# Optimization experiments

Hardware: AMD Instinct MI355X
Metric: run time of the kernel (lower is better)

## Reference

```python
import jax, jax.numpy as jnp
import numpy as np

RADII = (0.4, 0.8, 1.2)
SIGMA2 = 2.0 * 0.2 ** 2   # Gaussian shell-density bandwidth
ALPHA = 0.3               # keras LeakyReLU default
EPS = 1e-3                # keras BatchNormalization default epsilon


def _n_coeffs(L):
    return sum((2 * l + 1) ** 2 for l in range(L + 1))


def _pullback_idx(L):
    # flat index of Wigner block entry (m, n=0) for each SH coeff (l, m)
    idx, off = [], 0
    for l in range(L + 1):
        d = 2 * l + 1
        idx += [off + m * d + l for m in range(d)]
        off += d * d
    return np.asarray(idx, dtype=np.int32)


def setup_inputs() -> dict:
    key = jax.random.key(0)
    ks = jax.random.split(key, 20)
    B, N, Q, S = 64, 2048, 1024, 512
    T = [_n_coeffs(l) for l in (5, 4, 3)]  # 286, 165, 84
    f32 = jnp.float32

    def nrm(k, shape, scale=1.0):
        return jax.random.normal(ks[k], shape, dtype=f32) * scale

    dirs = nrm(1, (3, S, 3))
    dirs = dirs / jnp.linalg.norm(dirs, axis=-1, keepdims=True)
    z = lambda n: jnp.zeros((n,), f32)
    o = lambda n: jnp.ones((n,), f32)
    return {
        "x": nrm(0, (B, N, 3)),
        "shell_dirs": dirs,                                   # [3, 512, 3]
        "A_sh": nrm(2, (36, S), 1.0 / np.sqrt(S)),            # SH projection (l_max=5)
        "D_eval0": nrm(3, (Q, T[0]), 1.0 / np.sqrt(T[0])),    # Wigner eval bases
        "D_eval1": nrm(4, (Q, T[1]), 1.0 / np.sqrt(T[1])),
        "D_eval2": nrm(5, (Q, T[2]), 1.0 / np.sqrt(T[2])),
        "D_coef1": nrm(6, (T[1], Q), 1.0 / np.sqrt(Q)),       # Wigner coeff (projection) bases
        "D_coef2": nrm(7, (T[2], Q), 1.0 / np.sqrt(Q)),
        "D_coef_last": nrm(8, (T[2], Q), 1.0 / np.sqrt(Q)),
        "W0": nrm(9, (3, 16), 1.0 / np.sqrt(3)), "b0": z(16),
        "W1": nrm(10, (16, 32), 0.25), "b1": z(32),
        "W2": nrm(11, (32, 64), 1.0 / np.sqrt(32)), "b2": z(64),
        "g0": o(16), "be0": z(16),
        "g1": o(32), "be1": z(32),
        "g2": o(64), "be2": z(64),
        "Wfc1": nrm(12, (256, 512), 1.0 / 16.0), "bfc1": z(512),
        "gfc1": o(512), "befc1": z(512),
        "Wfc2": nrm(13, (512, 256), 1.0 / np.sqrt(512)), "bfc2": z(256),
        "gfc2": o(256), "befc2": z(256),
        "Wout": nrm(14, (256, 40), 1.0 / 16.0), "bout": z(40),
    }


def _bn(y, g, b, axes):
    m = jnp.mean(y, axis=axes, keepdims=True)
    v = jnp.var(y, axis=axes, keepdims=True)
    return (y - m) * jax.lax.rsqrt(v + EPS) * g + b


def reference(x, shell_dirs, A_sh, D_eval0, D_eval1, D_eval2,
              D_coef1, D_coef2, D_coef_last,
              W0, b0, W1, b1, W2, b2,
              g0, be0, g1, be1, g2, be2,
              Wfc1, bfc1, gfc1, befc1, Wfc2, bfc2, gfc2, befc2,
              Wout, bout):
    B = x.shape[0]
    # --- sphere_shell_embedding: Gaussian shell density -> SH coeffs per shell ---
    xn2 = jnp.sum(x * x, -1)[..., None]                 # [B,N,1]
    sh = []
    for i, r in enumerate(RADII):
        c = r * shell_dirs[i]                           # [S,3]
        d2 = xn2 + jnp.sum(c * c, -1) - 2.0 * (x @ c.T)  # [B,N,S]
        f = jnp.mean(jnp.exp(-d2 / SIGMA2), axis=1)      # [B,S]
        sh.append(f @ A_sh.T)                            # [B,36]
    sh = jnp.stack(sh, axis=-1)                          # [B,36,3] shells as channels
    # --- S2_to_SO3_pullback: Y_lm -> D^l_{m,0} column of Wigner blocks ---
    idx = jnp.asarray(_pullback_idx(5))
    y = jnp.zeros((B, 286, 3), sh.dtype).at[:, idx, :].set(sh)
    # --- layer 0: SO3Conv (per-coeff channel mix) + WignerEval + BN + LReLU + WignerCoeffs ---
    y = jnp.einsum('btc,cu->btu', y, W0) + b0
    y = jnp.einsum('qt,btu->bqu', D_eval0, y)            # [B,1024,16]
    y = jax.nn.leaky_relu(_bn(y, g0, be0, (0, 1)), ALPHA)
    y = jnp.einsum('tq,bqu->btu', D_coef1, y)            # [B,165,16]
    # --- layer 1 ---
    y = jnp.einsum('btc,cu->btu', y, W1) + b1
    y = jnp.einsum('qt,btu->bqu', D_eval1, y)            # [B,1024,32]
    y = jax.nn.leaky_relu(_bn(y, g1, be1, (0, 1)), ALPHA)
    y = jnp.einsum('tq,bqu->btu', D_coef2, y)            # [B,84,32]
    # --- layer 2 ---
    y = jnp.einsum('btc,cu->btu', y, W2) + b2
    y = jnp.einsum('qt,btu->bqu', D_eval2, y)            # [B,1024,64]
    y = jax.nn.leaky_relu(_bn(y, g2, be2, (0, 1)), ALPHA)
    y = jnp.einsum('tq,bqu->btu', D_coef_last, y)        # [B,84,64]
    # --- degree-wise norms (rotation-invariant pooling), l_max=3 blocks ---
    offs, sizes = (0, 1, 10, 35), (1, 9, 25, 49)
    feats = jnp.concatenate(
        [jnp.linalg.norm(y[:, o:o + s, :], axis=1, keepdims=True)
         for o, s in zip(offs, sizes)], axis=1)          # [B,4,64]
    h = feats.reshape(B, -1)                             # [B,256]
    # --- MLP head (dropout = identity at inference) ---
    h = jax.nn.relu(_bn(h @ Wfc1 + bfc1, gfc1, befc1, (0,)))
    h = jax.nn.relu(_bn(h @ Wfc2 + bfc2, gfc2, befc2, (0,)))
    return jax.nn.softmax(h @ Wout + bout, axis=-1)
```

## Files before the change

### kernel.cpp

```cpp
#include <hip/hip_runtime.h>
#include <hip/hip_bf16.h>

#define BB 64
#define NN 2048
#define QQ 1024
#define SS 512
#define NCH 16
#define PREPB 609
#define QKN3 4

__device__ const int PIDX[36] = {
    0, 2, 5, 8, 12, 17, 22, 27, 32, 38, 45, 52, 59, 66, 73, 80,
    88, 97, 106, 115, 124, 133, 142, 151, 160,
    170, 181, 192, 203, 214, 225, 236, 247, 258, 269, 280};

__global__ __launch_bounds__(256) void k_preshell(
    const float* __restrict__ De0, const float* __restrict__ De1, const float* __restrict__ De2,
    float* __restrict__ Dg0t, float* __restrict__ rs0,
    float* __restrict__ Det1, float* __restrict__ Det2,
    float* __restrict__ stats,
    const float* __restrict__ x, const float* __restrict__ dirs, float* __restrict__ pbuf) {
    __shared__ float tile[32][33];
    __shared__ float4 lx[NN / NCH];
    int blk = blockIdx.x, tid = threadIdx.x;
    if (blk < PREPB) {
        int r = tid >> 5, c = tid & 31;
        if (blk < 192) {
            int tq = blk & 31, tt = blk >> 5;
            int q0 = tq * 32, t0 = tt * 32;
            for (int rr = r; rr < 32; rr += 8) {
                int t = t0 + c;
                tile[rr][c] = (t < 165) ? De1[(q0 + rr) * 165 + t] : 0.f;
            }
            __syncthreads();
            for (int rr = r; rr < 32; rr += 8) {
                int t = t0 + rr;
                if (t < 165) Det1[t * QQ + q0 + c] = tile[c][rr];
            }
        } else if (blk < 288) {
            int i = blk - 192;
            int tq = i & 31, tt = i >> 5;
            int q0 = tq * 32, t0 = tt * 32;
            for (int rr = r; rr < 32; rr += 8) {
                int t = t0 + c;
                tile[rr][c] = (t < 84) ? De2[(q0 + rr) * 84 + t] : 0.f;
            }
            __syncthreads();
            for (int rr = r; rr < 32; rr += 8) {
                int t = t0 + rr;
                if (t < 84) Det2[t * QQ + q0 + c] = tile[c][rr];
            }
        } else if (blk < 352) {
            int i = blk - 288;
            int tq = i & 31, tj = i >> 5;
            int q0 = tq * 32, j0 = tj * 32;
            for (int rr = r; rr < 32; rr += 8) {
                int j = j0 + c;
                tile[rr][c] = (j < 36) ? De0[(q0 + rr) * 286 + PIDX[j]] : 0.f;
            }
            __syncthreads();
            for (int rr = r; rr < 32; rr += 8) {
                int j = j0 + rr;
                if (j < 36) Dg0t[j * QQ + q0 + c] = tile[c][rr];
            }
        } else if (blk < 608) {
            int w = tid >> 6, lane = tid & 63;
            int q = (blk - 352) * 4 + w;
            float s = 0.f;
#pragma unroll
            for (int p = 0; p < 5; p++) {
                int idx = lane + p * 64;
                if (idx < 286) s += De0[q * 286 + idx];
            }
#pragma unroll
            for (int o = 32; o > 0; o >>= 1) s += __shfl_xor(s, o, 64);
            if (lane == 0) rs0[q] = s;
        } else {
            if (tid < 224) stats[tid] = 0.f;
        }
        return;
    }
    int idx = blk - PREPB;
    int b = idx & 63, zc = idx >> 6;
    const float KL = 18.033688011112042f;
    const float* xb = x + ((size_t)b * NN + zc * (NN / NCH)) * 3;
    for (int n = tid; n < NN / NCH; n += 256) {
        float X = xb[n * 3 + 0];
        float Y = xb[n * 3 + 1];
        float Z = xb[n * 3 + 2];
        lx[n] = make_float4(X, Y, Z, -KL * (X * X + Y * Y + Z * Z));
    }
    __syncthreads();
    float cxs[3][2], cys[3][2], czs[3][2], bas[3][2];
#pragma unroll
    for (int i = 0; i < 3; i++) {
        float r = (i == 0) ? 0.4f : ((i == 1) ? 0.8f : 1.2f);
#pragma unroll
        for (int h = 0; h < 2; h++) {
            int s = tid + h * 256;
            float cx = r * dirs[(i * SS + s) * 3 + 0];
            float cy = r * dirs[(i * SS + s) * 3 + 1];
            float cz = r * dirs[(i * SS + s) * 3 + 2];
            bas[i][h] = -KL * (cx * cx + cy * cy + cz * cz);
            cxs[i][h] = 2.f * KL * cx;
            cys[i][h] = 2.f * KL * cy;
            czs[i][h] = 2.f * KL * cz;
        }
    }
    float acc[3][2];
#pragma unroll
    for (int i = 0; i < 3; i++) { acc[i][0] = 0.f; acc[i][1] = 0.f; }
#pragma unroll 4
    for (int n = 0; n < NN / NCH; n++) {
        float4 p = lx[n];
#pragma unroll
        for (int i = 0; i < 3; i++)
#pragma unroll
            for (int h = 0; h < 2; h++)
                acc[i][h] += __builtin_amdgcn_exp2f(
                    fmaf(cxs[i][h], p.x, fmaf(cys[i][h], p.y, fmaf(czs[i][h], p.z, p.w + bas[i][h]))));
    }
#pragma unroll
    for (int i = 0; i < 3; i++) {
        float* o = pbuf + ((size_t)(zc * 3 + i) * BB + b) * SS;
        o[tid] = acc[i][0];
        o[tid + 256] = acc[i][1];
    }
}

__global__ __launch_bounds__(256) void k_eval0(const float* __restrict__ pbuf,
                                               const float* __restrict__ A_sh,
                                               const float* __restrict__ W0,
                                               const float* __restrict__ b0,
                                               const float* __restrict__ Dg0t,
                                               const float* __restrict__ rs0,
                                               float* __restrict__ yq, float* __restrict__ stats) {
    __shared__ float lf[3][SS];
    __shared__ float lsh[36][3];
    __shared__ float llm[576];
    __shared__ float lred[4][32];
    int qc = blockIdx.x, b = blockIdx.y, tid = threadIdx.x;
    for (int i = tid; i < 3 * SS; i += 256) {
        int c = i / SS, s = i % SS;
        float v = 0.f;
#pragma unroll
        for (int zc = 0; zc < NCH; zc++) v += pbuf[((size_t)(zc * 3 + c) * BB + b) * SS + s];
        lf[c][s] = v * (1.0f / NN);
    }
    __syncthreads();
    int w = tid >> 6, lane = tid & 63;
    for (int p = w; p < 108; p += 4) {
        int j = p / 3, c = p % 3;
        const float* As = A_sh + j * SS;
        float a = 0.f;
#pragma unroll
        for (int k = 0; k < 8; k++) a = fmaf(lf[c][lane + 64 * k], As[lane + 64 * k], a);
#pragma unroll
        for (int o = 32; o > 0; o >>= 1) a += __shfl_xor(a, o, 64);
        if (lane == 0) lsh[j][c] = a;
    }
    __syncthreads();
    for (int i = tid; i < 576; i += 256) {
        int j = i >> 4, u = i & 15;
        float m = 0.f;
#pragma unroll
        for (int c = 0; c < 3; c++) m = fmaf(lsh[j][c], W0[c * 16 + u], m);
        llm[i] = m;
    }
    __syncthreads();
    int q = qc * 256 + tid;
    float acc[16];
#pragma unroll
    for (int u = 0; u < 16; u++) acc[u] = 0.f;
#pragma unroll 4
    for (int j = 0; j < 36; j++) {
        float d = Dg0t[j * QQ + q];
#pragma unroll
        for (int u = 0; u < 16; u++) acc[u] = fmaf(d, llm[j * 16 + u], acc[u]);
    }
    float rb = rs0[q];
#pragma unroll
    for (int u = 0; u < 16; u++) acc[u] = fmaf(b0[u], rb, acc[u]);
#pragma unroll
    for (int u = 0; u < 16; u++) yq[((size_t)b * 16 + u) * QQ + q] = acc[u];
#pragma unroll
    for (int u = 0; u < 16; u++) {
        float v = acc[u], v2 = acc[u] * acc[u];
#pragma unroll
        for (int o = 32; o > 0; o >>= 1) {
            v += __shfl_xor(v, o, 64);
            v2 += __shfl_xor(v2, o, 64);
        }
        if (lane == 0) { lred[w][u] = v; lred[w][16 + u] = v2; }
    }
    __syncthreads();
    if (tid < 32) atomicAdd(&stats[tid], lred[0][tid] + lred[1][tid] + lred[2][tid] + lred[3][tid]);
}

template <int TT, int UU, int QKN>
__global__ __launch_bounds__(256) void k_coefG(const float* __restrict__ yq,
                                               const float* __restrict__ Dc,
                                               const float* __restrict__ stats,
                                               const float* __restrict__ g,
                                               const float* __restrict__ be,
                                               float* __restrict__ part) {
    constexpr int KC = QQ / QKN;
    __shared__ float lA[32][68];
    __shared__ float lB[32][68];
    __shared__ float lsu[UU], ltu[UU];
    int mt = blockIdx.x, nt = blockIdx.y, qk = blockIdx.z, tid = threadIdx.x;
    int m0 = mt * 64, n0 = nt * 64, k0 = qk * KC;
    if (tid < UU) {
        const float inv = 1.0f / (BB * QQ);
        float mm = stats[tid] * inv;
        float var = stats[UU + tid] * inv - mm * mm;
        float s = g[tid] * rsqrtf(fmaxf(var, 0.f) + 1e-3f);
        lsu[tid] = s;
        ltu[tid] = be[tid] - mm * s;
    }
    __syncthreads();
    int r = tid >> 2;
    int f = (tid & 3) * 4;
    bool mok = (m0 + r) < TT;
    const float* arow = Dc + (size_t)(mok ? (m0 + r) : 0) * QQ;
    const float* brow = yq + (size_t)(n0 + r) * QQ;
    float su = lsu[(n0 + r) % UU], tu = ltu[(n0 + r) % UU];
    int tg = tid >> 4, ug = tid & 15;
    float acc[4][4];
#pragma unroll
    for (int i = 0; i < 4; i++)
#pragma unroll
        for (int j = 0; j < 4; j++) acc[i][j] = 0.f;
    for (int kb = 0; kb < KC; kb += 32) {
        int kg = k0 + kb;
#pragma unroll
        for (int p = 0; p < 2; p++) {
            int ko = f + p * 16;
            float4 a4 = make_float4(0.f, 0.f, 0.f, 0.f);
            if (mok) a4 = *(const float4*)(arow + kg + ko);
            float4 b4 = *(const float4*)(brow + kg + ko);
#pragma unroll
            for (int i = 0; i < 4; i++) {
                float v = fmaf((&b4.x)[i], su, tu);
                lA[ko + i][r] = (&a4.x)[i];
                lB[ko + i][r] = (v > 0.f) ? v : 0.3f * v;
            }
        }
        __syncthreads();
#pragma unroll 2
        for (int kk = 0; kk < 32; kk++) {
            float4 a4 = *(const float4*)&lA[kk][tg * 4];
            float4 b4 = *(const float4*)&lB[kk][ug * 4];
#pragma unroll
            for (int i = 0; i < 4; i++) {
                float av = (&a4.x)[i];
                acc[i][0] = fmaf(av, b4.x, acc[i][0]);
                acc[i][1] = fmaf(av, b4.y, acc[i][1]);
                acc[i][2] = fmaf(av, b4.z, acc[i][2]);
                acc[i][3] = fmaf(av, b4.w, acc[i][3]);
            }
        }
        __syncthreads();
    }
    int n = n0 + ug * 4;
    int b = n / UU, u0 = n % UU;
#pragma unroll
    for (int i = 0; i < 4; i++) {
        int t = m0 + tg * 4 + i;
        if (t < TT)
            *(float4*)&part[(((size_t)qk * BB + b) * TT + t) * UU + u0] =
                make_float4(acc[i][0], acc[i][1], acc[i][2], acc[i][3]);
    }
}

template <int TT, int CC, int UU, int QKN, int TTp>
__global__ __launch_bounds__(256) void k_redmix(const float* __restrict__ part,
                                                const float* __restrict__ W,
                                                const float* __restrict__ bias,
                                                float* __restrict__ ym) {
    constexpr int CCp = CC + 1;
    __shared__ float lyt[TT * CCp];
    int b = blockIdx.x, tid = threadIdx.x;
    for (int i = tid; i < TT * CC; i += 256) {
        float v = 0.f;
#pragma unroll
        for (int k = 0; k < QKN; k++) v += part[(size_t)k * (BB * TT * CC) + (size_t)b * TT * CC + i];
        lyt[(i / CC) * CCp + (i % CC)] = v;
    }
    __syncthreads();
    for (int i = tid; i < UU * TTp; i += 256) {
        int u = i / TTp, t = i % TTp;
        float m = 0.f;
        if (t < TT) {
            m = bias[u];
#pragma unroll
            for (int c = 0; c < CC; c++) m = fmaf(lyt[t * CCp + c], W[c * UU + u], m);
        }
        ym[((size_t)b * UU + u) * TTp + t] = m;
    }
}

template <int TT, int TTp, int UU>
__global__ __launch_bounds__(256) void k_evalG(const float* __restrict__ ym,
                                               const float* __restrict__ Det,
                                               float* __restrict__ yq,
                                               float* __restrict__ stats) {
    __shared__ float lA[32][68];
    __shared__ float lB[32][68];
    __shared__ float sred[2][64];
    int mt = blockIdx.x, qt = blockIdx.y, tid = threadIdx.x;
    int m0 = mt * 64, q0 = qt * 64;
    int r = tid >> 2, f = (tid & 3) * 4;
    const float* arow = ym + (size_t)(m0 + r) * TTp;
    int br = tid >> 4, bq = (tid & 15) * 4;
    int tg = tid >> 4, ug = tid & 15;
    float acc[4][4];
#pragma unroll
    for (int i = 0; i < 4; i++)
#pragma unroll
        for (int j = 0; j < 4; j++) acc[i][j] = 0.f;
    for (int kb = 0; kb < TT; kb += 32) {
#pragma unroll
        for (int p = 0; p < 2; p++) {
            int ko = f + p * 16;
            float4 a4 = *(const float4*)(arow + kb + ko);
#pragma unroll
            for (int i = 0; i < 4; i++) lA[ko + i][r] = (&a4.x)[i];
            int kk = br + p * 16;
            int t = kb + kk;
            float4 b4 = make_float4(0.f, 0.f, 0.f, 0.f);
            if (t < TT) b4 = *(const float4*)(Det + (size_t)t * QQ + q0 + bq);
            *(float4*)&lB[kk][bq] = b4;
        }
        __syncthreads();
#pragma unroll 2
        for (int kk = 0; kk < 32; kk++) {
            float4 a4 = *(const float4*)&lA[kk][tg * 4];
            float4 b4 = *(const float4*)&lB[kk][ug * 4];
#pragma unroll
            for (int i = 0; i < 4; i++) {
                float av = (&a4.x)[i];
                acc[i][0] = fmaf(av, b4.x, acc[i][0]);
                acc[i][1] = fmaf(av, b4.y, acc[i][1]);
                acc[i][2] = fmaf(av, b4.z, acc[i][2]);
                acc[i][3] = fmaf(av, b4.w, acc[i][3]);
            }
        }
        __syncthreads();
    }
    float s1[4], s2[4];
#pragma unroll
    for (int i = 0; i < 4; i++) {
        int m = m0 + tg * 4 + i;
        *(float4*)&yq[(size_t)m * QQ + q0 + ug * 4] =
            make_float4(acc[i][0], acc[i][1], acc[i][2], acc[i][3]);
        s1[i] = (acc[i][0] + acc[i][1]) + (acc[i][2] + acc[i][3]);
        s2[i] = fmaf(acc[i][0], acc[i][0], fmaf(acc[i][1], acc[i][1],
                 fmaf(acc[i][2], acc[i][2], acc[i][3] * acc[i][3])));
    }
#pragma unroll
    for (int o = 1; o < 16; o <<= 1) {
#pragma unroll
        for (int i = 0; i < 4; i++) {
            s1[i] += __shfl_xor(s1[i], o, 64);
            s2[i] += __shfl_xor(s2[i], o, 64);
        }
    }
    if (ug == 0) {
#pragma unroll
        for (int i = 0; i < 4; i++) {
            sred[0][tg * 4 + i] = s1[i];
            sred[1][tg * 4 + i] = s2[i];
        }
    }
    __syncthreads();
    if (tid < 2 * UU) {
        int which = tid / UU, u = tid % UU;
        float s = 0.f;
        for (int rr = u; rr < 64; rr += UU) s += sred[which][rr];
        atomicAdd(&stats[which * UU + u], s);
    }
}

__global__ __launch_bounds__(256) void k_norms(const float* __restrict__ part, float* __restrict__ ht0) {
    __shared__ float ly[84 * 64];
    int b = blockIdx.x, tid = threadIdx.x;
    for (int i = tid; i < 84 * 64; i += 256) {
        float v = 0.f;
#pragma unroll
        for (int k = 0; k < QKN3; k++) v += part[(size_t)k * (BB * 84 * 64) + b * (84 * 64) + i];
        ly[i] = v;
    }
    __syncthreads();
    int blk = tid >> 6, u = tid & 63;
    const int offs[4] = {0, 1, 10, 35};
    const int ends[4] = {1, 10, 35, 84};
    float a = 0.f;
    for (int t = offs[blk]; t < ends[blk]; t++) {
        float v = ly[t * 64 + u];
        a = fmaf(v, v, a);
    }
    ht0[(blk * 64 + u) * BB + b] = sqrtf(fmaxf(a, 0.f));
}

template <int K, int J>
__global__ __launch_bounds__(512) void k_fc(const float* __restrict__ in, const float* __restrict__ W,
                                            const float* __restrict__ bias, const float* __restrict__ g,
                                            const float* __restrict__ be, float* __restrict__ out) {
    __shared__ float red[8][64];
    int j = blockIdx.x;
    int b = threadIdx.x & 63, kq = threadIdx.x >> 6;
    constexpr int KS = K / 8;
    int kbeg = kq * KS;
    float a0 = 0.f, a1 = 0.f, a2 = 0.f, a3 = 0.f;
#pragma unroll 4
    for (int k = kbeg; k < kbeg + KS; k += 4) {
        a0 = fmaf(in[k * BB + b], W[(size_t)k * J + j], a0);
        a1 = fmaf(in[(k + 1) * BB + b], W[(size_t)(k + 1) * J + j], a1);
        a2 = fmaf(in[(k + 2) * BB + b], W[(size_t)(k + 2) * J + j], a2);
        a3 = fmaf(in[(k + 3) * BB + b], W[(size_t)(k + 3) * J + j], a3);
    }
    red[kq][b] = (a0 + a1) + (a2 + a3);
    __syncthreads();
    if (kq == 0) {
        float acc = bias[j];
#pragma unroll
        for (int i = 0; i < 8; i++) acc += red[i][b];
        float s1 = acc, s2 = acc * acc;
#pragma unroll
        for (int o = 32; o > 0; o >>= 1) {
            s1 += __shfl_xor(s1, o, 64);
            s2 += __shfl_xor(s2, o, 64);
        }
        float m = s1 * (1.0f / 64.f);
        float var = s2 * (1.0f / 64.f) - m * m;
        float sc = g[j] * rsqrtf(fmaxf(var, 0.f) + 1e-3f);
        float v = (acc - m) * sc + be[j];
        out[j * BB + b] = fmaxf(v, 0.f);
    }
}

__global__ __launch_bounds__(256) void k_out(const float* __restrict__ ht2, const float* __restrict__ Wout,
                                             const float* __restrict__ bout, float* __restrict__ outp) {
    __shared__ float red[4][64];
    __shared__ float sm[64];
    int b = blockIdx.x;
    int o = threadIdx.x & 63, kq = threadIdx.x >> 6;
    float a0 = 0.f, a1 = 0.f, a2 = 0.f, a3 = 0.f;
    int kbeg = kq * 64;
    if (o < 40) {
#pragma unroll 4
        for (int k = kbeg; k < kbeg + 64; k += 4) {
            a0 = fmaf(ht2[k * BB + b], Wout[k * 40 + o], a0);
            a1 = fmaf(ht2[(k + 1) * BB + b], Wout[(k + 1) * 40 + o], a1);
            a2 = fmaf(ht2[(k + 2) * BB + b], Wout[(k + 2) * 40 + o], a2);
            a3 = fmaf(ht2[(k + 3) * BB + b], Wout[(k + 3) * 40 + o], a3);
        }
    }
    red[kq][o] = (a0 + a1) + (a2 + a3);
    __syncthreads();
    if (kq == 0) {
        float acc = red[0][o] + red[1][o] + red[2][o] + red[3][o] + ((o < 40) ? bout[o] : 0.f);
        sm[o] = (o < 40) ? acc : -3.0e38f;
        __syncthreads();
        for (int s = 32; s > 0; s >>= 1) {
            if (o < s) sm[o] = fmaxf(sm[o], sm[o + s]);
            __syncthreads();
        }
        float m = sm[0];
        __syncthreads();
        const float L2E = 1.4426950408889634f;
        float e = (o < 40) ? exp2f((acc - m) * L2E) : 0.f;
        sm[o] = e;
        __syncthreads();
        for (int s = 32; s > 0; s >>= 1) {
            if (o < s) sm[o] += sm[o + s];
            __syncthreads();
        }
        if (o < 40) outp[b * 40 + o] = e / sm[0];
    }
}

#define OFF_PBUF 0
#define OFF_DG0T 1572864
#define OFF_RS0 1609728
#define OFF_DET1 1610752
#define OFF_DET2 1779712
#define OFF_YQ 1865728
#define OFF_YM 6060032
#define OFF_HT0 6453248
#define OFF_HT1 6469632
#define OFF_HT2 6502400
#define OFF_STATS 6518784

extern "C" void kernel_launch(void* const* d_in, const int* in_sizes, int n_in,
                              void* d_out, int out_size, void* d_ws, size_t ws_size,
                              hipStream_t stream) {
    const float* x = (const float*)d_in[0];
    const float* shell_dirs = (const float*)d_in[1];
    const float* A_sh = (const float*)d_in[2];
    const float* D_eval0 = (const float*)d_in[3];
    const float* D_eval1 = (const float*)d_in[4];
    const float* D_eval2 = (const float*)d_in[5];
    const float* D_coef1 = (const float*)d_in[6];
    const float* D_coef2 = (const float*)d_in[7];
    const float* D_coef_last = (const float*)d_in[8];
    const float* W0 = (const float*)d_in[9];
    const float* b0 = (const float*)d_in[10];
    const float* W1 = (const float*)d_in[11];
    const float* b1 = (const float*)d_in[12];
    const float* W2 = (const float*)d_in[13];
    const float* b2 = (const float*)d_in[14];
    const float* g0 = (const float*)d_in[15];
    const float* be0 = (const float*)d_in[16];
    const float* g1 = (const float*)d_in[17];
    const float* be1 = (const float*)d_in[18];
    const float* g2 = (const float*)d_in[19];
    const float* be2 = (const float*)d_in[20];
    const float* Wfc1 = (const float*)d_in[21];
    const float* bfc1 = (const float*)d_in[22];
    const float* gfc1 = (const float*)d_in[23];
    const float* befc1 = (const float*)d_in[24];
    const float* Wfc2 = (const float*)d_in[25];
    const float* bfc2 = (const float*)d_in[26];
    const float* gfc2 = (const float*)d_in[27];
    const float* befc2 = (const float*)d_in[28];
    const float* Wout = (const float*)d_in[29];
    const float* bout = (const float*)d_in[30];
    float* out = (float*)d_out;

    float* ws = (float*)d_ws;
    float* pbuf = ws + OFF_PBUF;
    float* part = ws + OFF_PBUF;
    float* Dg0t = ws + OFF_DG0T;
    float* rs0 = ws + OFF_RS0;
    float* Det1 = ws + OFF_DET1;
    float* Det2 = ws + OFF_DET2;
    float* yq = ws + OFF_YQ;
    float* ym = ws + OFF_YM;
    float* ht0 = ws + OFF_HT0;
    float* ht1 = ws + OFF_HT1;
    float* ht2 = ws + OFF_HT2;
    float* stats = ws + OFF_STATS;
    float* stats0 = stats;
    float* stats1 = stats + 32;
    float* stats2 = stats + 96;

    k_preshell<<<PREPB + BB * NCH, 256, 0, stream>>>(
        D_eval0, D_eval1, D_eval2, Dg0t, rs0, Det1, Det2, stats, x, shell_dirs, pbuf);
    k_eval0<<<dim3(4, BB), 256, 0, stream>>>(pbuf, A_sh, W0, b0, Dg0t, rs0, yq, stats0);
    k_coefG<165, 16, 8><<<dim3(3, 16, 8), 256, 0, stream>>>(yq, D_coef1, stats0, g0, be0, part);
    k_redmix<165, 16, 32, 8, 192><<<BB, 256, 0, stream>>>(part, W1, b1, ym);
    k_evalG<165, 192, 32><<<dim3(32, 16), 256, 0, stream>>>(ym, Det1, yq, stats1);
    k_coefG<84, 32, 8><<<dim3(2, 32, 8), 256, 0, stream>>>(yq, D_coef2, stats1, g1, be1, part);
    k_redmix<84, 32, 64, 8, 96><<<BB, 256, 0, stream>>>(part, W2, b2, ym);
    k_evalG<84, 96, 64><<<dim3(64, 16), 256, 0, stream>>>(ym, Det2, yq, stats2);
    k_coefG<84, 64, QKN3><<<dim3(2, 64, QKN3), 256, 0, stream>>>(yq, D_coef_last, stats2, g2, be2, part);
    k_norms<<<BB, 256, 0, stream>>>(part, ht0);
    k_fc<256, 512><<<512, 512, 0, stream>>>(ht0, Wfc1, bfc1, gfc1, befc1, ht1);
    k_fc<512, 256><<<256, 512, 0, stream>>>(ht1, Wfc2, bfc2, gfc2, befc2, ht2);
    k_out<<<BB, 256, 0, stream>>>(ht2, Wout, bout, out);
}
```

Before: 353.5 us.

## Fuse all stages into a persistent megakernel with software grid barriers

Replaces the chain of thirteen kernel launches with one persistent kernel of 512 blocks. Each stage loops over its former block indices with a grid-stride loop, and stages are separated by an atomic-counter grid barrier in workspace, reset by a memset before launch. This removes per-launch overhead and inter-kernel gaps. In exchange it adds barrier spin cost, assumes all 512 blocks are co-resident, and forces every stage to run on a fixed grid, which may underfill or serialize some stages.

```diff
diff --git a/kernel.cpp b/kernel.cpp
--- a/kernel.cpp
+++ b/kernel.cpp
@@ -6,209 +6,50 @@
 #define QQ 1024
 #define SS 512
 #define NCH 16
-#define PREPB 609
-#define QKN3 4
+#define GRID 512
 
 __device__ const int PIDX[36] = {
     0, 2, 5, 8, 12, 17, 22, 27, 32, 38, 45, 52, 59, 66, 73, 80,
     88, 97, 106, 115, 124, 133, 142, 151, 160,
     170, 181, 192, 203, 214, 225, 236, 247, 258, 269, 280};
 
-__global__ __launch_bounds__(256) void k_preshell(
-    const float* __restrict__ De0, const float* __restrict__ De1, const float* __restrict__ De2,
-    float* __restrict__ Dg0t, float* __restrict__ rs0,
-    float* __restrict__ Det1, float* __restrict__ Det2,
-    float* __restrict__ stats,
-    const float* __restrict__ x, const float* __restrict__ dirs, float* __restrict__ pbuf) {
-    __shared__ float tile[32][33];
-    __shared__ float4 lx[NN / NCH];
-    int blk = blockIdx.x, tid = threadIdx.x;
-    if (blk < PREPB) {
-        int r = tid >> 5, c = tid & 31;
-        if (blk < 192) {
-            int tq = blk & 31, tt = blk >> 5;
-            int q0 = tq * 32, t0 = tt * 32;
-            for (int rr = r; rr < 32; rr += 8) {
-                int t = t0 + c;
-                tile[rr][c] = (t < 165) ? De1[(q0 + rr) * 165 + t] : 0.f;
-            }
-            __syncthreads();
-            for (int rr = r; rr < 32; rr += 8) {
-                int t = t0 + rr;
-                if (t < 165) Det1[t * QQ + q0 + c] = tile[c][rr];
-            }
-        } else if (blk < 288) {
-            int i = blk - 192;
-            int tq = i & 31, tt = i >> 5;
-            int q0 = tq * 32, t0 = tt * 32;
-            for (int rr = r; rr < 32; rr += 8) {
-                int t = t0 + c;
-                tile[rr][c] = (t < 84) ? De2[(q0 + rr) * 84 + t] : 0.f;
-            }
-            __syncthreads();
-            for (int rr = r; rr < 32; rr += 8) {
-                int t = t0 + rr;
-                if (t < 84) Det2[t * QQ + q0 + c] = tile[c][rr];
-            }
-        } else if (blk < 352) {
-            int i = blk - 288;
-            int tq = i & 31, tj = i >> 5;
-            int q0 = tq * 32, j0 = tj * 32;
-            for (int rr = r; rr < 32; rr += 8) {
-                int j = j0 + c;
-                tile[rr][c] = (j < 36) ? De0[(q0 + rr) * 286 + PIDX[j]] : 0.f;
-            }
-            __syncthreads();
-            for (int rr = r; rr < 32; rr += 8) {
-                int j = j0 + rr;
-                if (j < 36) Dg0t[j * QQ + q0 + c] = tile[c][rr];
-            }
-        } else if (blk < 608) {
-            int w = tid >> 6, lane = tid & 63;
-            int q = (blk - 352) * 4 + w;
-            float s = 0.f;
-#pragma unroll
-            for (int p = 0; p < 5; p++) {
-                int idx = lane + p * 64;
-                if (idx < 286) s += De0[q * 286 + idx];
-            }
-#pragma unroll
-            for (int o = 32; o > 0; o >>= 1) s += __shfl_xor(s, o, 64);
-            if (lane == 0) rs0[q] = s;
+struct Args {
+    const float *x, *dirs, *A_sh, *De0, *De1, *De2, *Dc1, *Dc2, *Dc3;
+    const float *W0, *b0, *W1, *b1, *W2, *b2;
+    const float *g0, *be0, *g1, *be1, *g2, *be2;
+    const float *Wfc1, *bfc1, *gfc1, *befc1, *Wfc2, *bfc2, *gfc2, *befc2, *Wout, *bout;
+    float *Dg0t, *rs0, *Det1, *Det2, *pbuf, *yq, *part, *ym, *ht0, *ht1, *ht2, *stats, *out;
+    unsigned* bar;
+};
+
+__device__ __forceinline__ void gbar(unsigned* bar) {
+    __syncthreads();
+    if (threadIdx.x == 0) {
+        __threadfence();
+        unsigned g = __hip_atomic_load(&bar[1], __ATOMIC_RELAXED, __HIP_MEMORY_SCOPE_AGENT);
+        unsigned arr = __hip_atomic_fetch_add(&bar[0], 1u, __ATOMIC_ACQ_REL, __HIP_MEMORY_SCOPE_AGENT);
+        if (arr == GRID - 1) {
+            __hip_atomic_store(&bar[0], 0u, __ATOMIC_RELAXED, __HIP_MEMORY_SCOPE_AGENT);
+            __hip_atomic_fetch_add(&bar[1], 1u, __ATOMIC_RELEASE, __HIP_MEMORY_SCOPE_AGENT);
         } else {
-            if (tid < 224) stats[tid] = 0.f;
-        }
-        return;
-    }
-    int idx = blk - PREPB;
-    int b = idx & 63, zc = idx >> 6;
-    const float KL = 18.033688011112042f;
-    const float* xb = x + ((size_t)b * NN + zc * (NN / NCH)) * 3;
-    for (int n = tid; n < NN / NCH; n += 256) {
-        float X = xb[n * 3 + 0];
-        float Y = xb[n * 3 + 1];
-        float Z = xb[n * 3 + 2];
-        lx[n] = make_float4(X, Y, Z, -KL * (X * X + Y * Y + Z * Z));
+            while (__hip_atomic_load(&bar[1], __ATOMIC_RELAXED, __HIP_MEMORY_SCOPE_AGENT) == g)
+                __builtin_amdgcn_s_sleep(2);
+        }
+        (void)__hip_atomic_load(&bar[1], __ATOMIC_ACQUIRE, __HIP_MEMORY_SCOPE_AGENT);
     }
     __syncthreads();
-    float cxs[3][2], cys[3][2], czs[3][2], bas[3][2];
-#pragma unroll
-    for (int i = 0; i < 3; i++) {
-        float r = (i == 0) ? 0.4f : ((i == 1) ? 0.8f : 1.2f);
-#pragma unroll
-        for (int h = 0; h < 2; h++) {
-            int s = tid + h * 256;
-            float cx = r * dirs[(i * SS + s) * 3 + 0];
-            float cy = r * dirs[(i * SS + s) * 3 + 1];
-            float cz = r * dirs[(i * SS + s) * 3 + 2];
-            bas[i][h] = -KL * (cx * cx + cy * cy + cz * cz);
-            cxs[i][h] = 2.f * KL * cx;
-            cys[i][h] = 2.f * KL * cy;
-            czs[i][h] = 2.f * KL * cz;
-        }
-    }
-    float acc[3][2];
-#pragma unroll
-    for (int i = 0; i < 3; i++) { acc[i][0] = 0.f; acc[i][1] = 0.f; }
-#pragma unroll 4
-    for (int n = 0; n < NN / NCH; n++) {
-        float4 p = lx[n];
-#pragma unroll
-        for (int i = 0; i < 3; i++)
-#pragma unroll
-            for (int h = 0; h < 2; h++)
-                acc[i][h] += __builtin_amdgcn_exp2f(
-                    fmaf(cxs[i][h], p.x, fmaf(cys[i][h], p.y, fmaf(czs[i][h], p.z, p.w + bas[i][h]))));
-    }
-#pragma unroll
-    for (int i = 0; i < 3; i++) {
-        float* o = pbuf + ((size_t)(zc * 3 + i) * BB + b) * SS;
-        o[tid] = acc[i][0];
-        o[tid + 256] = acc[i][1];
-    }
 }
 
-__global__ __launch_bounds__(256) void k_eval0(const float* __restrict__ pbuf,
-                                               const float* __restrict__ A_sh,
-                                               const float* __restrict__ W0,
-                                               const float* __restrict__ b0,
-                                               const float* __restrict__ Dg0t,
-                                               const float* __restrict__ rs0,
-                                               float* __restrict__ yq, float* __restrict__ stats) {
-    __shared__ float lf[3][SS];
-    __shared__ float lsh[36][3];
-    __shared__ float llm[576];
-    __shared__ float lred[4][32];
-    int qc = blockIdx.x, b = blockIdx.y, tid = threadIdx.x;
-    for (int i = tid; i < 3 * SS; i += 256) {
-        int c = i / SS, s = i % SS;
-        float v = 0.f;
-#pragma unroll
-        for (int zc = 0; zc < NCH; zc++) v += pbuf[((size_t)(zc * 3 + c) * BB + b) * SS + s];
-        lf[c][s] = v * (1.0f / NN);
-    }
-    __syncthreads();
-    int w = tid >> 6, lane = tid & 63;
-    for (int p = w; p < 108; p += 4) {
-        int j = p / 3, c = p % 3;
-        const float* As = A_sh + j * SS;
-        float a = 0.f;
-#pragma unroll
-        for (int k = 0; k < 8; k++) a = fmaf(lf[c][lane + 64 * k], As[lane + 64 * k], a);
-#pragma unroll
-        for (int o = 32; o > 0; o >>= 1) a += __shfl_xor(a, o, 64);
-        if (lane == 0) lsh[j][c] = a;
-    }
-    __syncthreads();
-    for (int i = tid; i < 576; i += 256) {
-        int j = i >> 4, u = i & 15;
-        float m = 0.f;
-#pragma unroll
-        for (int c = 0; c < 3; c++) m = fmaf(lsh[j][c], W0[c * 16 + u], m);
-        llm[i] = m;
-    }
-    __syncthreads();
-    int q = qc * 256 + tid;
-    float acc[16];
-#pragma unroll
-    for (int u = 0; u < 16; u++) acc[u] = 0.f;
-#pragma unroll 4
-    for (int j = 0; j < 36; j++) {
-        float d = Dg0t[j * QQ + q];
-#pragma unroll
-        for (int u = 0; u < 16; u++) acc[u] = fmaf(d, llm[j * 16 + u], acc[u]);
-    }
-    float rb = rs0[q];
-#pragma unroll
-    for (int u = 0; u < 16; u++) acc[u] = fmaf(b0[u], rb, acc[u]);
-#pragma unroll
-    for (int u = 0; u < 16; u++) yq[((size_t)b * 16 + u) * QQ + q] = acc[u];
-#pragma unroll
-    for (int u = 0; u < 16; u++) {
-        float v = acc[u], v2 = acc[u] * acc[u];
-#pragma unroll
-        for (int o = 32; o > 0; o >>= 1) {
-            v += __shfl_xor(v, o, 64);
-            v2 += __shfl_xor(v2, o, 64);
-        }
-        if (lane == 0) { lred[w][u] = v; lred[w][16 + u] = v2; }
-    }
-    __syncthreads();
-    if (tid < 32) atomicAdd(&stats[tid], lred[0][tid] + lred[1][tid] + lred[2][tid] + lred[3][tid]);
-}
-
 template <int TT, int UU, int QKN>
-__global__ __launch_bounds__(256) void k_coefG(const float* __restrict__ yq,
-                                               const float* __restrict__ Dc,
-                                               const float* __restrict__ stats,
-                                               const float* __restrict__ g,
-                                               const float* __restrict__ be,
-                                               float* __restrict__ part) {
+__device__ __forceinline__ void coef_unit(float* smem, int mt, int nt, int qk, const Args& a,
+                                          const float* Dc, const float* stats,
+                                          const float* g, const float* be) {
     constexpr int KC = QQ / QKN;
-    __shared__ float lA[32][68];
-    __shared__ float lB[32][68];
-    __shared__ float lsu[UU], ltu[UU];
-    int mt = blockIdx.x, nt = blockIdx.y, qk = blockIdx.z, tid = threadIdx.x;
+    float* lA = smem;
+    float* lB = smem + 2176;
+    float* lsu = smem + 4352;
+    float* ltu = smem + 4352 + UU;
+    int tid = threadIdx.x;
     int m0 = mt * 64, n0 = nt * 64, k0 = qk * KC;
     if (tid < UU) {
         const float inv = 1.0f / (BB * QQ);
@@ -219,11 +60,10 @@
         ltu[tid] = be[tid] - mm * s;
     }
     __syncthreads();
-    int r = tid >> 2;
-    int f = (tid & 3) * 4;
+    int r = tid >> 2, f = (tid & 3) * 4;
     bool mok = (m0 + r) < TT;
     const float* arow = Dc + (size_t)(mok ? (m0 + r) : 0) * QQ;
-    const float* brow = yq + (size_t)(n0 + r) * QQ;
+    const float* brow = a.yq + (size_t)(n0 + r) * QQ;
     float su = lsu[(n0 + r) % UU], tu = ltu[(n0 + r) % UU];
     int tg = tid >> 4, ug = tid & 15;
     float acc[4][4];
@@ -242,15 +82,15 @@
 #pragma unroll
             for (int i = 0; i < 4; i++) {
                 float v = fmaf((&b4.x)[i], su, tu);
-                lA[ko + i][r] = (&a4.x)[i];
-                lB[ko + i][r] = (v > 0.f) ? v : 0.3f * v;
+                lA[(ko + i) * 68 + r] = (&a4.x)[i];
+                lB[(ko + i) * 68 + r] = (v > 0.f) ? v : 0.3f * v;
             }
         }
         __syncthreads();
 #pragma unroll 2
         for (int kk = 0; kk < 32; kk++) {
-            float4 a4 = *(const float4*)&lA[kk][tg * 4];
-            float4 b4 = *(const float4*)&lB[kk][ug * 4];
+            float4 a4 = *(const float4*)&lA[kk * 68 + tg * 4];
+            float4 b4 = *(const float4*)&lB[kk * 68 + ug * 4];
 #pragma unroll
             for (int i = 0; i < 4; i++) {
                 float av = (&a4.x)[i];
@@ -268,23 +108,21 @@
     for (int i = 0; i < 4; i++) {
         int t = m0 + tg * 4 + i;
         if (t < TT)
-            *(float4*)&part[(((size_t)qk * BB + b) * TT + t) * UU + u0] =
+            *(float4*)&a.part[(((size_t)qk * BB + b) * TT + t) * UU + u0] =
                 make_float4(acc[i][0], acc[i][1], acc[i][2], acc[i][3]);
     }
 }
 
 template <int TT, int CC, int UU, int QKN, int TTp>
-__global__ __launch_bounds__(256) void k_redmix(const float* __restrict__ part,
-                                                const float* __restrict__ W,
-                                                const float* __restrict__ bias,
-                                                float* __restrict__ ym) {
+__device__ __forceinline__ void redmix_unit(float* smem, int b, const Args& a,
+                                            const float* W, const float* bias) {
     constexpr int CCp = CC + 1;
-    __shared__ float lyt[TT * CCp];
-    int b = blockIdx.x, tid = threadIdx.x;
+    float* lyt = smem;
+    int tid = threadIdx.x;
     for (int i = tid; i < TT * CC; i += 256) {
         float v = 0.f;
 #pragma unroll
-        for (int k = 0; k < QKN; k++) v += part[(size_t)k * (BB * TT * CC) + (size_t)b * TT * CC + i];
+        for (int k = 0; k < QKN; k++) v += a.part[(size_t)k * (BB * TT * CC) + (size_t)b * TT * CC + i];
         lyt[(i / CC) * CCp + (i % CC)] = v;
     }
     __syncthreads();
@@ -296,22 +134,20 @@
 #pragma unroll
             for (int c = 0; c < CC; c++) m = fmaf(lyt[t * CCp + c], W[c * UU + u], m);
         }
-        ym[((size_t)b * UU + u) * TTp + t] = m;
+        a.ym[((size_t)b * UU + u) * TTp + t] = m;
     }
 }
 
 template <int TT, int TTp, int UU>
-__global__ __launch_bounds__(256) void k_evalG(const float* __restrict__ ym,
-                                               const float* __restrict__ Det,
-                                               float* __restrict__ yq,
-                                               float* __restrict__ stats) {
-    __shared__ float lA[32][68];
-    __shared__ float lB[32][68];
-    __shared__ float sred[2][64];
-    int mt = blockIdx.x, qt = blockIdx.y, tid = threadIdx.x;
+__device__ __forceinline__ void evalG_unit(float* smem, int mt, int qt, const Args& a,
+                                           const float* Det, float* stats) {
+    float* lA = smem;
+    float* lB = smem + 2176;
+    float* sred = smem + 4352;
+    int tid = threadIdx.x;
     int m0 = mt * 64, q0 = qt * 64;
     int r = tid >> 2, f = (tid & 3) * 4;
-    const float* arow = ym + (size_t)(m0 + r) * TTp;
+    const float* arow = a.ym + (size_t)(m0 + r) * TTp;
     int br = tid >> 4, bq = (tid & 15) * 4;
     int tg = tid >> 4, ug = tid & 15;
     float acc[4][4];
@@ -325,18 +161,18 @@
             int ko = f + p * 16;
             float4 a4 = *(const float4*)(arow + kb + ko);
 #pragma unroll
-            for (int i = 0; i < 4; i++) lA[ko + i][r] = (&a4.x)[i];
+            for (int i = 0; i < 4; i++) lA[(ko + i) * 68 + r] = (&a4.x)[i];
             int kk = br + p * 16;
             int t = kb + kk;
             float4 b4 = make_float4(0.f, 0.f, 0.f, 0.f);
             if (t < TT) b4 = *(const float4*)(Det + (size_t)t * QQ + q0 + bq);
-            *(float4*)&lB[kk][bq] = b4;
+            *(float4*)&lB[kk * 68 + bq] = b4;
         }
         __syncthreads();
 #pragma unroll 2
         for (int kk = 0; kk < 32; kk++) {
-            float4 a4 = *(const float4*)&lA[kk][tg * 4];
-            float4 b4 = *(const float4*)&lB[kk][ug * 4];
+            float4 a4 = *(const float4*)&lA[kk * 68 + tg * 4];
+            float4 b4 = *(const float4*)&lB[kk * 68 + ug * 4];
 #pragma unroll
             for (int i = 0; i < 4; i++) {
                 float av = (&a4.x)[i];
@@ -352,7 +188,7 @@
 #pragma unroll
     for (int i = 0; i < 4; i++) {
         int m = m0 + tg * 4 + i;
-        *(float4*)&yq[(size_t)m * QQ + q0 + ug * 4] =
+        *(float4*)&a.yq[(size_t)m * QQ + q0 + ug * 4] =
             make_float4(acc[i][0], acc[i][1], acc[i][2], acc[i][3]);
         s1[i] = (acc[i][0] + acc[i][1]) + (acc[i][2] + acc[i][3]);
         s2[i] = fmaf(acc[i][0], acc[i][0], fmaf(acc[i][1], acc[i][1],
@@ -369,48 +205,26 @@
     if (ug == 0) {
 #pragma unroll
         for (int i = 0; i < 4; i++) {
-            sred[0][tg * 4 + i] = s1[i];
-            sred[1][tg * 4 + i] = s2[i];
+            sred[tg * 4 + i] = s1[i];
+            sred[64 + tg * 4 + i] = s2[i];
         }
     }
     __syncthreads();
     if (tid < 2 * UU) {
         int which = tid / UU, u = tid % UU;
         float s = 0.f;
-        for (int rr = u; rr < 64; rr += UU) s += sred[which][rr];
+        for (int rr = u; rr < 64; rr += UU) s += sred[which * 64 + rr];
         atomicAdd(&stats[which * UU + u], s);
     }
 }
 
-__global__ __launch_bounds__(256) void k_norms(const float* __restrict__ part, float* __restrict__ ht0) {
-    __shared__ float ly[84 * 64];
-    int b = blockIdx.x, tid = threadIdx.x;
-    for (int i = tid; i < 84 * 64; i += 256) {
-        float v = 0.f;
-#pragma unroll
-        for (int k = 0; k < QKN3; k++) v += part[(size_t)k * (BB * 84 * 64) + b * (84 * 64) + i];
-        ly[i] = v;
-    }
-    __syncthreads();
-    int blk = tid >> 6, u = tid & 63;
-    const int offs[4] = {0, 1, 10, 35};
-    const int ends[4] = {1, 10, 35, 84};
-    float a = 0.f;
-    for (int t = offs[blk]; t < ends[blk]; t++) {
-        float v = ly[t * 64 + u];
-        a = fmaf(v, v, a);
-    }
-    ht0[(blk * 64 + u) * BB + b] = sqrtf(fmaxf(a, 0.f));
-}
-
 template <int K, int J>
-__global__ __launch_bounds__(512) void k_fc(const float* __restrict__ in, const float* __restrict__ W,
-                                            const float* __restrict__ bias, const float* __restrict__ g,
-                                            const float* __restrict__ be, float* __restrict__ out) {
-    __shared__ float red[8][64];
-    int j = blockIdx.x;
+__device__ __forceinline__ void fc_unit(float* smem, int j, const float* in, const float* W,
+                                        const float* bias, const float* g, const float* be,
+                                        float* out) {
+    float* red = smem;
     int b = threadIdx.x & 63, kq = threadIdx.x >> 6;
-    constexpr int KS = K / 8;
+    constexpr int KS = K / 4;
     int kbeg = kq * KS;
     float a0 = 0.f, a1 = 0.f, a2 = 0.f, a3 = 0.f;
 #pragma unroll 4
@@ -420,12 +234,10 @@
         a2 = fmaf(in[(k + 2) * BB + b], W[(size_t)(k + 2) * J + j], a2);
         a3 = fmaf(in[(k + 3) * BB + b], W[(size_t)(k + 3) * J + j], a3);
     }
-    red[kq][b] = (a0 + a1) + (a2 + a3);
+    red[kq * 64 + b] = (a0 + a1) + (a2 + a3);
     __syncthreads();
     if (kq == 0) {
-        float acc = bias[j];
-#pragma unroll
-        for (int i = 0; i < 8; i++) acc += red[i][b];
+        float acc = red[b] + red[64 + b] + red[128 + b] + red[192 + b] + bias[j];
         float s1 = acc, s2 = acc * acc;
 #pragma unroll
         for (int o = 32; o > 0; o >>= 1) {
@@ -440,44 +252,305 @@
     }
 }
 
-__global__ __launch_bounds__(256) void k_out(const float* __restrict__ ht2, const float* __restrict__ Wout,
-                                             const float* __restrict__ bout, float* __restrict__ outp) {
-    __shared__ float red[4][64];
-    __shared__ float sm[64];
-    int b = blockIdx.x;
-    int o = threadIdx.x & 63, kq = threadIdx.x >> 6;
-    float a0 = 0.f, a1 = 0.f, a2 = 0.f, a3 = 0.f;
-    int kbeg = kq * 64;
-    if (o < 40) {
+__global__ __launch_bounds__(256) void k_mega(Args a) {
+    __shared__ __align__(16) float smem[5632];
+    const int tid = threadIdx.x;
+    const float KL = 18.033688011112042f;
+
+    for (int u = blockIdx.x; u < 1633; u += GRID) {
+        int r = tid >> 5, c = tid & 31;
+        if (u < 192) {
+            int tq = u & 31, tt = u >> 5;
+            int q0 = tq * 32, t0 = tt * 32;
+            for (int rr = r; rr < 32; rr += 8) {
+                int t = t0 + c;
+                smem[rr * 33 + c] = (t < 165) ? a.De1[(q0 + rr) * 165 + t] : 0.f;
+            }
+            __syncthreads();
+            for (int rr = r; rr < 32; rr += 8) {
+                int t = t0 + rr;
+                if (t < 165) a.Det1[t * QQ + q0 + c] = smem[c * 33 + rr];
+            }
+        } else if (u < 288) {
+            int i = u - 192;
+            int tq = i & 31, tt = i >> 5;
+            int q0 = tq * 32, t0 = tt * 32;
+            for (int rr = r; rr < 32; rr += 8) {
+                int t = t0 + c;
+                smem[rr * 33 + c] = (t < 84) ? a.De2[(q0 + rr) * 84 + t] : 0.f;
+            }
+            __syncthreads();
+            for (int rr = r; rr < 32; rr += 8) {
+                int t = t0 + rr;
+                if (t < 84) a.Det2[t * QQ + q0 + c] = smem[c * 33 + rr];
+            }
+        } else if (u < 352) {
+            int i = u - 288;
+            int tq = i & 31, tj = i >> 5;
+            int q0 = tq * 32, j0 = tj * 32;
+            for (int rr = r; rr < 32; rr += 8) {
+                int j = j0 + c;
+                smem[rr * 33 + c] = (j < 36) ? a.De0[(q0 + rr) * 286 + PIDX[j]] : 0.f;
+            }
+            __syncthreads();
+            for (int rr = r; rr < 32; rr += 8) {
+                int j = j0 + rr;
+                if (j < 36) a.Dg0t[j * QQ + q0 + c] = smem[c * 33 + rr];
+            }
+        } else if (u < 608) {
+            int w = tid >> 6, lane = tid & 63;
+            int q = (u - 352) * 4 + w;
+            float s = 0.f;
+#pragma unroll
+            for (int p = 0; p < 5; p++) {
+                int idx = lane + p * 64;
+                if (idx < 286) s += a.De0[q * 286 + idx];
+            }
+#pragma unroll
+            for (int o = 32; o > 0; o >>= 1) s += __shfl_xor(s, o, 64);
+            if (lane == 0) a.rs0[q] = s;
+        } else if (u == 608) {
+            if (tid < 224) a.stats[tid] = 0.f;
+        } else {
+            int idx = u - 609;
+            int b = idx & 63, zc = idx >> 6;
+            float4* lx = (float4*)smem;
+            const float* xb = a.x + ((size_t)b * NN + zc * (NN / NCH)) * 3;
+            for (int n = tid; n < NN / NCH; n += 256) {
+                float X = xb[n * 3 + 0], Y = xb[n * 3 + 1], Z = xb[n * 3 + 2];
+                lx[n] = make_float4(X, Y, Z, -KL * (X * X + Y * Y + Z * Z));
+            }
+            __syncthreads();
+            float cxs[3][2], cys[3][2], czs[3][2], bas[3][2];
+#pragma unroll
+            for (int i = 0; i < 3; i++) {
+                float rr = (i == 0) ? 0.4f : ((i == 1) ? 0.8f : 1.2f);
+#pragma unroll
+                for (int h = 0; h < 2; h++) {
+                    int s = tid + h * 256;
+                    float cx = rr * a.dirs[(i * SS + s) * 3 + 0];
+                    float cy = rr * a.dirs[(i * SS + s) * 3 + 1];
+                    float cz = rr * a.dirs[(i * SS + s) * 3 + 2];
+                    bas[i][h] = -KL * (cx * cx + cy * cy + cz * cz);
+                    cxs[i][h] = 2.f * KL * cx;
+                    cys[i][h] = 2.f * KL * cy;
+                    czs[i][h] = 2.f * KL * cz;
+                }
+            }
+            float acc[3][2];
+#pragma unroll
+            for (int i = 0; i < 3; i++) { acc[i][0] = 0.f; acc[i][1] = 0.f; }
 #pragma unroll 4
-        for (int k = kbeg; k < kbeg + 64; k += 4) {
-            a0 = fmaf(ht2[k * BB + b], Wout[k * 40 + o], a0);
-            a1 = fmaf(ht2[(k + 1) * BB + b], Wout[(k + 1) * 40 + o], a1);
-            a2 = fmaf(ht2[(k + 2) * BB + b], Wout[(k + 2) * 40 + o], a2);
-            a3 = fmaf(ht2[(k + 3) * BB + b], Wout[(k + 3) * 40 + o], a3);
-        }
-    }
-    red[kq][o] = (a0 + a1) + (a2 + a3);
-    __syncthreads();
-    if (kq == 0) {
-        float acc = red[0][o] + red[1][o] + red[2][o] + red[3][o] + ((o < 40) ? bout[o] : 0.f);
-        sm[o] = (o < 40) ? acc : -3.0e38f;
+            for (int n = 0; n < NN / NCH; n++) {
+                float4 p = lx[n];
+#pragma unroll
+                for (int i = 0; i < 3; i++)
+#pragma unroll
+                    for (int h = 0; h < 2; h++)
+                        acc[i][h] += __builtin_amdgcn_exp2f(
+                            fmaf(cxs[i][h], p.x,
+                                 fmaf(cys[i][h], p.y, fmaf(czs[i][h], p.z, p.w + bas[i][h]))));
+            }
+#pragma unroll
+            for (int i = 0; i < 3; i++) {
+                float* o = a.pbuf + ((size_t)(zc * 3 + i) * BB + b) * SS;
+                o[tid] = acc[i][0];
+                o[tid + 256] = acc[i][1];
+            }
+        }
+        __syncthreads();
+    }
+    gbar(a.bar);
+
+    for (int u = blockIdx.x; u < 256; u += GRID) {
+        int qc = u & 3, b = u >> 2;
+        float* lf = smem;
+        float* lsh = smem + 1536;
+        float* llm = smem + 1648;
+        float* lred = smem + 2240;
+        for (int i = tid; i < 3 * SS; i += 256) {
+            int c = i / SS, s = i % SS;
+            float v = 0.f;
+#pragma unroll
+            for (int zc = 0; zc < NCH; zc++) v += a.pbuf[((size_t)(zc * 3 + c) * BB + b) * SS + s];
+            lf[c * SS + s] = v * (1.0f / NN);
+        }
+        __syncthreads();
+        int w = tid >> 6, lane = tid & 63;
+        for (int p = w; p < 108; p += 4) {
+            int j = p / 3, c = p % 3;
+            const float* As = a.A_sh + j * SS;
+            float aa = 0.f;
+#pragma unroll
+            for (int k = 0; k < 8; k++) aa = fmaf(lf[c * SS + lane + 64 * k], As[lane + 64 * k], aa);
+#pragma unroll
+            for (int o = 32; o > 0; o >>= 1) aa += __shfl_xor(aa, o, 64);
+            if (lane == 0) lsh[j * 3 + c] = aa;
+        }
+        __syncthreads();
+        for (int i = tid; i < 576; i += 256) {
+            int j = i >> 4, uu = i & 15;
+            float m = 0.f;
+#pragma unroll
+            for (int c = 0; c < 3; c++) m = fmaf(lsh[j * 3 + c], a.W0[c * 16 + uu], m);
+            llm[i] = m;
+        }
+        __syncthreads();
+        int q = qc * 256 + tid;
+        float acc[16];
+#pragma unroll
+        for (int uu = 0; uu < 16; uu++) acc[uu] = 0.f;
+#pragma unroll 4
+        for (int j = 0; j < 36; j++) {
+            float d = a.Dg0t[j * QQ + q];
+#pragma unroll
+            for (int uu = 0; uu < 16; uu++) acc[uu] = fmaf(d, llm[j * 16 + uu], acc[uu]);
+        }
+        float rb = a.rs0[q];
+#pragma unroll
+        for (int uu = 0; uu < 16; uu++) acc[uu] = fmaf(a.b0[uu], rb, acc[uu]);
+#pragma unroll
+        for (int uu = 0; uu < 16; uu++) a.yq[((size_t)b * 16 + uu) * QQ + q] = acc[uu];
+#pragma unroll
+        for (int uu = 0; uu < 16; uu++) {
+            float v = acc[uu], v2 = acc[uu] * acc[uu];
+#pragma unroll
+            for (int o = 32; o > 0; o >>= 1) {
+                v += __shfl_xor(v, o, 64);
+                v2 += __shfl_xor(v2, o, 64);
+            }
+            if (lane == 0) { lred[w * 32 + uu] = v; lred[w * 32 + 16 + uu] = v2; }
+        }
+        __syncthreads();
+        if (tid < 32)
+            atomicAdd(&a.stats[tid], lred[tid] + lred[32 + tid] + lred[64 + tid] + lred[96 + tid]);
+        __syncthreads();
+    }
+    gbar(a.bar);
+
+    for (int u = blockIdx.x; u < 384; u += GRID) {
+        int mt = u / 128, rem = u % 128;
+        coef_unit<165, 16, 8>(smem, mt, rem / 8, rem % 8, a, a.Dc1, a.stats, a.g0, a.be0);
+        __syncthreads();
+    }
+    gbar(a.bar);
+
+    for (int u = blockIdx.x; u < 64; u += GRID) {
+        redmix_unit<165, 16, 32, 8, 192>(smem, u, a, a.W1, a.b1);
+        __syncthreads();
+    }
+    gbar(a.bar);
+
+    for (int u = blockIdx.x; u < 512; u += GRID) {
+        evalG_unit<165, 192, 32>(smem, u & 31, u >> 5, a, a.Det1, a.stats + 32);
+        __syncthreads();
+    }
+    gbar(a.bar);
+
+    for (int u = blockIdx.x; u < 512; u += GRID) {
+        int mt = u / 256, rem = u % 256;
+        coef_unit<84, 32, 8>(smem, mt, rem / 8, rem % 8, a, a.Dc2, a.stats + 32, a.g1, a.be1);
+        __syncthreads();
+    }
+    gbar(a.bar);
+
+    for (int u = blockIdx.x; u < 64; u += GRID) {
+        redmix_unit<84, 32, 64, 8, 96>(smem, u, a, a.W2, a.b2);
+        __syncthreads();
+    }
+    gbar(a.bar);
+
+    for (int u = blockIdx.x; u < 1024; u += GRID) {
+        evalG_unit<84, 96, 64>(smem, u & 63, u >> 6, a, a.Det2, a.stats + 96);
+        __syncthreads();
+    }
+    gbar(a.bar);
+
+    for (int u = blockIdx.x; u < 512; u += GRID) {
+        int mt = u / 256, rem = u % 256;
+        coef_unit<84, 64, 4>(smem, mt, rem / 4, rem % 4, a, a.Dc3, a.stats + 96, a.g2, a.be2);
+        __syncthreads();
+    }
+    gbar(a.bar);
+
+    for (int u = blockIdx.x; u < 64; u += GRID) {
+        int b = u;
+        float* ly = smem;
+        for (int i = tid; i < 84 * 64; i += 256) {
+            float v = 0.f;
+#pragma unroll
+            for (int k = 0; k < 4; k++) v += a.part[(size_t)k * (BB * 84 * 64) + b * (84 * 64) + i];
+            ly[i] = v;
+        }
+        __syncthreads();
+        int blk = tid >> 6, uu = tid & 63;
+        const int offs[4] = {0, 1, 10, 35};
+        const int ends[4] = {1, 10, 35, 84};
+        float aa = 0.f;
+        for (int t = offs[blk]; t < ends[blk]; t++) {
+            float v = ly[t * 64 + uu];
+            aa = fmaf(v, v, aa);
+        }
+        a.ht0[(blk * 64 + uu) * BB + b] = sqrtf(fmaxf(aa, 0.f));
+        __syncthreads();
+    }
+    gbar(a.bar);
+
+    for (int u = blockIdx.x; u < 512; u += GRID) {
+        fc_unit<256, 512>(smem, u, a.ht0, a.Wfc1, a.bfc1, a.gfc1, a.befc1, a.ht1);
+        __syncthreads();
+    }
+    gbar(a.bar);
+
+    for (int u = blockIdx.x; u < 256; u += GRID) {
+        fc_unit<512, 256>(smem, u, a.ht1, a.Wfc2, a.bfc2, a.gfc2, a.befc2, a.ht2);
+        __syncthreads();
+    }
+    gbar(a.bar);
+
+    for (int u = blockIdx.x; u < 64; u += GRID) {
+        int b = u;
+        float* red = smem;
+        float* sm = smem + 256;
+        int o = tid & 63, kq = tid >> 6;
+        float a0 = 0.f, a1 = 0.f, a2 = 0.f, a3 = 0.f;
+        int kbeg = kq * 64;
+        if (o < 40) {
+#pragma unroll 4
+            for (int k = kbeg; k < kbeg + 64; k += 4) {
+                a0 = fmaf(a.ht2[k * BB + b], a.Wout[k * 40 + o], a0);
+                a1 = fmaf(a.ht2[(k + 1) * BB + b], a.Wout[(k + 1) * 40 + o], a1);
+                a2 = fmaf(a.ht2[(k + 2) * BB + b], a.Wout[(k + 2) * 40 + o], a2);
+                a3 = fmaf(a.ht2[(k + 3) * BB + b], a.Wout[(k + 3) * 40 + o], a3);
+            }
+        }
+        red[kq * 64 + o] = (a0 + a1) + (a2 + a3);
+        __syncthreads();
+        float acc = 0.f;
+        if (kq == 0) {
+            acc = red[o] + red[64 + o] + red[128 + o] + red[192 + o] + ((o < 40) ? a.bout[o] : 0.f);
+            sm[o] = (o < 40) ? acc : -3.0e38f;
+        }
         __syncthreads();
         for (int s = 32; s > 0; s >>= 1) {
-            if (o < s) sm[o] = fmaxf(sm[o], sm[o + s]);
+            if (tid < s) sm[tid] = fmaxf(sm[tid], sm[tid + s]);
             __syncthreads();
         }
         float m = sm[0];
         __syncthreads();
         const float L2E = 1.4426950408889634f;
-        float e = (o < 40) ? exp2f((acc - m) * L2E) : 0.f;
-        sm[o] = e;
+        float e = 0.f;
+        if (kq == 0) {
+            e = (o < 40) ? exp2f((acc - m) * L2E) : 0.f;
+            sm[o] = e;
+        }
         __syncthreads();
         for (int s = 32; s > 0; s >>= 1) {
-            if (o < s) sm[o] += sm[o + s];
+            if (tid < s) sm[tid] += sm[tid + s];
             __syncthreads();
         }
-        if (o < 40) outp[b * 40 + o] = e / sm[0];
+        if (kq == 0 && o < 40) a.out[b * 40 + o] = e / sm[0];
+        __syncthreads();
     }
 }
 
@@ -492,72 +565,59 @@
 #define OFF_HT1 6469632
 #define OFF_HT2 6502400
 #define OFF_STATS 6518784
+#define OFF_BAR 6519040
 
 extern "C" void kernel_launch(void* const* d_in, const int* in_sizes, int n_in,
                               void* d_out, int out_size, void* d_ws, size_t ws_size,
                               hipStream_t stream) {
-    const float* x = (const float*)d_in[0];
-    const float* shell_dirs = (const float*)d_in[1];
-    const float* A_sh = (const float*)d_in[2];
-    const float* D_eval0 = (const float*)d_in[3];
-    const float* D_eval1 = (const float*)d_in[4];
-    const float* D_eval2 = (const float*)d_in[5];
-    const float* D_coef1 = (const float*)d_in[6];
-    const float* D_coef2 = (const float*)d_in[7];
-    const float* D_coef_last = (const float*)d_in[8];
-    const float* W0 = (const float*)d_in[9];
-    const float* b0 = (const float*)d_in[10];
-    const float* W1 = (const float*)d_in[11];
-    const float* b1 = (const float*)d_in[12];
-    const float* W2 = (const float*)d_in[13];
-    const float* b2 = (const float*)d_in[14];
-    const float* g0 = (const float*)d_in[15];
-    const float* be0 = (const float*)d_in[16];
-    const float* g1 = (const float*)d_in[17];
-    const float* be1 = (const float*)d_in[18];
-    const float* g2 = (const float*)d_in[19];
-    const float* be2 = (const float*)d_in[20];
-    const float* Wfc1 = (const float*)d_in[21];
-    const float* bfc1 = (const float*)d_in[22];
-    const float* gfc1 = (const float*)d_in[23];
-    const float* befc1 = (const float*)d_in[24];
-    const float* Wfc2 = (const float*)d_in[25];
-    const float* bfc2 = (const float*)d_in[26];
-    const float* gfc2 = (const float*)d_in[27];
-    const float* befc2 = (const float*)d_in[28];
-    const float* Wout = (const float*)d_in[29];
-    const float* bout = (const float*)d_in[30];
-    float* out = (float*)d_out;
-
     float* ws = (float*)d_ws;
-    float* pbuf = ws + OFF_PBUF;
-    float* part = ws + OFF_PBUF;
-    float* Dg0t = ws + OFF_DG0T;
-    float* rs0 = ws + OFF_RS0;
-    float* Det1 = ws + OFF_DET1;
-    float* Det2 = ws + OFF_DET2;
-    float* yq = ws + OFF_YQ;
-    float* ym = ws + OFF_YM;
-    float* ht0 = ws + OFF_HT0;
-    float* ht1 = ws + OFF_HT1;
-    float* ht2 = ws + OFF_HT2;
-    float* stats = ws + OFF_STATS;
-    float* stats0 = stats;
-    float* stats1 = stats + 32;
-    float* stats2 = stats + 96;
-
-    k_preshell<<<PREPB + BB * NCH, 256, 0, stream>>>(
-        D_eval0, D_eval1, D_eval2, Dg0t, rs0, Det1, Det2, stats, x, shell_dirs, pbuf);
-    k_eval0<<<dim3(4, BB), 256, 0, stream>>>(pbuf, A_sh, W0, b0, Dg0t, rs0, yq, stats0);
-    k_coefG<165, 16, 8><<<dim3(3, 16, 8), 256, 0, stream>>>(yq, D_coef1, stats0, g0, be0, part);
-    k_redmix<165, 16, 32, 8, 192><<<BB, 256, 0, stream>>>(part, W1, b1, ym);
-    k_evalG<165, 192, 32><<<dim3(32, 16), 256, 0, stream>>>(ym, Det1, yq, stats1);
-    k_coefG<84, 32, 8><<<dim3(2, 32, 8), 256, 0, stream>>>(yq, D_coef2, stats1, g1, be1, part);
-    k_redmix<84, 32, 64, 8, 96><<<BB, 256, 0, stream>>>(part, W2, b2, ym);
-    k_evalG<84, 96, 64><<<dim3(64, 16), 256, 0, stream>>>(ym, Det2, yq, stats2);
-    k_coefG<84, 64, QKN3><<<dim3(2, 64, QKN3), 256, 0, stream>>>(yq, D_coef_last, stats2, g2, be2, part);
-    k_norms<<<BB, 256, 0, stream>>>(part, ht0);
-    k_fc<256, 512><<<512, 512, 0, stream>>>(ht0, Wfc1, bfc1, gfc1, befc1, ht1);
-    k_fc<512, 256><<<256, 512, 0, stream>>>(ht1, Wfc2, bfc2, gfc2, befc2, ht2);
-    k_out<<<BB, 256, 0, stream>>>(ht2, Wout, bout, out);
+    Args a;
+    a.x = (const float*)d_in[0];
+    a.dirs = (const float*)d_in[1];
+    a.A_sh = (const float*)d_in[2];
+    a.De0 = (const float*)d_in[3];
+    a.De1 = (const float*)d_in[4];
+    a.De2 = (const float*)d_in[5];
+    a.Dc1 = (const float*)d_in[6];
+    a.Dc2 = (const float*)d_in[7];
+    a.Dc3 = (const float*)d_in[8];
+    a.W0 = (const float*)d_in[9];
+    a.b0 = (const float*)d_in[10];
+    a.W1 = (const float*)d_in[11];
+    a.b1 = (const float*)d_in[12];
+    a.W2 = (const float*)d_in[13];
+    a.b2 = (const float*)d_in[14];
+    a.g0 = (const float*)d_in[15];
+    a.be0 = (const float*)d_in[16];
+    a.g1 = (const float*)d_in[17];
+    a.be1 = (const float*)d_in[18];
+    a.g2 = (const float*)d_in[19];
+    a.be2 = (const float*)d_in[20];
+    a.Wfc1 = (const float*)d_in[21];
+    a.bfc1 = (const float*)d_in[22];
+    a.gfc1 = (const float*)d_in[23];
+    a.befc1 = (const float*)d_in[24];
+    a.Wfc2 = (const float*)d_in[25];
+    a.bfc2 = (const float*)d_in[26];
+    a.gfc2 = (const float*)d_in[27];
+    a.befc2 = (const float*)d_in[28];
+    a.Wout = (const float*)d_in[29];
+    a.bout = (const float*)d_in[30];
+    a.Dg0t = ws + OFF_DG0T;
+    a.rs0 = ws + OFF_RS0;
+    a.Det1 = ws + OFF_DET1;
+    a.Det2 = ws + OFF_DET2;
+    a.pbuf = ws + OFF_PBUF;
+    a.yq = ws + OFF_YQ;
+    a.part = ws + OFF_PBUF;
+    a.ym = ws + OFF_YM;
+    a.ht0 = ws + OFF_HT0;
+    a.ht1 = ws + OFF_HT1;
+    a.ht2 = ws + OFF_HT2;
+    a.stats = ws + OFF_STATS;
+    a.out = (float*)d_out;
+    a.bar = (unsigned*)(ws + OFF_BAR);
+
+    hipMemsetAsync(ws + OFF_BAR, 0, 2 * sizeof(unsigned), stream);
+    k_mega<<<GRID, 256, 0, stream>>>(a);
 }
```

Result: slower. 995.3 us (+181.6%).
